# Performance work log

Hardware: AMD Instinct MI355X
Metric: run time of the kernel (lower is better)

Reference implementation:

```python
import jax, jax.numpy as jnp
import numpy as np

EPS = 1e-6

def _ln(x, w, b):
    m = x.mean(-1, keepdims=True)
    v = ((x - m) ** 2).mean(-1, keepdims=True)
    return (x - m) / jnp.sqrt(v + EPS) * w + b

def setup_inputs() -> dict:
    key = jax.random.key(0)
    ks = jax.random.split(key, 16)
    N, P, C, M = 8192, 64, 128, 4096
    MW = M * P  # 262144 gathered tokens
    A, BL = 131072, 65536
    x = jax.random.normal(ks[0], (N, P, C), dtype=jnp.float32)
    index_window = jax.random.permutation(ks[1], N)[:M]
    index_partition = jax.random.permutation(ks[2], MW)
    perm2 = jax.random.permutation(ks[3], MW)
    asy_index = perm2[:A]
    blocked_index = perm2[A:A + BL]
    p = lambda k, sh: 0.02 * jax.random.normal(k, sh, dtype=jnp.float32)
    return {
        "x": x,
        "index_window": index_window,
        "index_partition": index_partition,
        "asy_index": asy_index,
        "blocked_index": blocked_index,
        "M": M,
        "B": N,
        "ln1_w": jnp.ones((C,), jnp.float32), "ln1_b": jnp.zeros((C,), jnp.float32),
        "qkv_w": p(ks[4], (C, 3 * C)), "qkv_b": jnp.zeros((3 * C,), jnp.float32),
        "proj_w": p(ks[5], (C, C)), "proj_b": jnp.zeros((C,), jnp.float32),
        "gamma1": jnp.full((C,), 1e-1, jnp.float32),
        "ln2_w": jnp.ones((C,), jnp.float32), "ln2_b": jnp.zeros((C,), jnp.float32),
        "mlp_w1": p(ks[6], (C, 4 * C)), "mlp_b1": jnp.zeros((4 * C,), jnp.float32),
        "mlp_w2": p(ks[7], (4 * C, C)), "mlp_b2": jnp.zeros((C,), jnp.float32),
        "gamma2": jnp.full((C,), 1e-1, jnp.float32),
    }

def reference(x, index_window, index_partition, asy_index, blocked_index, M, B,
              ln1_w, ln1_b, qkv_w, qkv_b, proj_w, proj_b, gamma1,
              ln2_w, ln2_b, mlp_w1, mlp_b1, mlp_w2, mlp_b2, gamma2):
    N, P, C = x.shape
    H, dh = 4, 32
    scale = dh ** -0.5
    MW = index_partition.shape[0]
    x = _ln(x, ln1_w, ln1_b)                      # first_norm over whole input
    X = x                                          # (N, P, C)
    xw = x[index_window].reshape(-1, C)            # gather windows -> (MW, C)
    XX = xw
    xa = _ln(xw[asy_index], ln1_w, ln1_b)          # second norm on asy tokens
    xw = xw.at[asy_index].set(xa)
    shortcut = xa                                  # (A, C)
    xp = xw[index_partition].reshape(M, -1, C)     # (M, P, C) attention groups
    qkv = (xp @ qkv_w + qkv_b).reshape(M, P, H, 3 * dh).transpose(0, 2, 1, 3)
    q, k, v = jnp.split(qkv, 3, axis=3)            # each (M, H, P, dh)
    attn = jnp.einsum('mhqd,mhkd->mhqk', q, k) * scale
    # scatter scores keyed by key-token into flat map, mask blocked keys, gather back
    am = jnp.zeros((MW, P, H), attn.dtype)
    am = am.at[index_partition].set(jnp.transpose(attn, (0, 3, 2, 1)).reshape(MW, P, H))
    am = am.at[blocked_index].set(-10000.0)
    attn = jnp.transpose(am[index_partition].reshape(M, P, P, H), (0, 3, 2, 1))
    attn = jax.nn.softmax(attn, axis=-1)
    o = jnp.einsum('mhqk,mhkd->mhqd', attn, v).transpose(0, 2, 1, 3).reshape(M, P, C)
    o = o @ proj_w + proj_b
    XX = XX.at[index_partition].set(o.reshape(-1, C))
    y = XX[asy_index]
    # sub_layers: [ls1, droppath(id), ln2, mlp, ls2, droppath(id)]
    y = y * gamma1                                 # i=0
    y = shortcut + y                               # i=1 residual
    shortcut = y
    y2 = _ln(y, ln2_w, ln2_b)                      # i=2
    y2 = jax.nn.gelu(y2 @ mlp_w1 + mlp_b1, approximate=False) @ mlp_w2 + mlp_b2  # i=3
    y2 = y2 * gamma2                               # i=4
    y = shortcut + y2                              # i=5 residual
    XX = XX.at[asy_index].set(y)
    XX = XX.at[blocked_index].set(X[index_window].reshape(-1, C)[blocked_index])
    X = X.at[index_window].set(XX.reshape(M, -1, C))
    return X
```

## Files before the change

kernel.cpp:

```cpp
#include <hip/hip_runtime.h>
#include <hip/hip_bf16.h>
#include <math.h>

#define N_   8192
#define P_   64
#define C_   128
#define M_   4096
#define MW_  (M_ * P_)
#define A_   131072
#define BL_  65536
#define NROWS_ (N_ * P_)
#define LNBLK_   (NROWS_ / 8)
#define PREPBLK_ (196608 / 256)
#define SETBLK_  (MW_ / 256)

typedef __attribute__((ext_vector_type(8))) __bf16 bf16x8;
typedef __attribute__((ext_vector_type(4))) __bf16 bf16x4;
typedef __attribute__((ext_vector_type(4))) float f32x4;
typedef __attribute__((ext_vector_type(2))) __bf16 bf16x2;

__device__ __forceinline__ float wave_sum(float v) {
#pragma unroll
  for (int o = 32; o > 0; o >>= 1) v += __shfl_xor(v, o, 64);
  return v;
}
__device__ __forceinline__ float half_sum(float v) {
#pragma unroll
  for (int o = 1; o < 32; o <<= 1) v += __shfl_xor(v, o, 64);
  return v;
}

__global__ __launch_bounds__(256) void k_scatter2(unsigned char* p,
                                                  const int* __restrict__ ia,
                                                  const int* __restrict__ ib) {
  int i = blockIdx.x * 256 + threadIdx.x;
  if (i < A_) p[ia[i]] = 1;
  else {
    int j = i - A_;
    if (j < BL_) p[ib[j]] = 2;
  }
}

__global__ __launch_bounds__(256) void k_ln_prep_set(
    const float* __restrict__ x,
    const float* __restrict__ w, const float* __restrict__ b,
    const float* __restrict__ qkvw, const float* __restrict__ projw,
    const float* __restrict__ w1, const float* __restrict__ w2,
    __bf16* __restrict__ qkvt, __bf16* __restrict__ projt,
    __bf16* __restrict__ w1t, __bf16* __restrict__ w2t,
    unsigned char* __restrict__ flags,
    float* __restrict__ out) {
  if (blockIdx.x >= LNBLK_) {
    int bx = blockIdx.x - LNBLK_;
    if (bx >= PREPBLK_) {
      int i = (bx - PREPBLK_) * 256 + threadIdx.x;
      flags[i] = 0;
      return;
    }
    int i = bx * 256 + threadIdx.x;
    if (i < 384 * 128) {
      int col = i >> 7, row = i & 127;
      qkvt[i] = (__bf16)qkvw[row * 384 + col];
    } else if (i < 384 * 128 + 128 * 128) {
      int j = i - 384 * 128;
      int col = j >> 7, row = j & 127;
      projt[j] = (__bf16)projw[row * 128 + col];
    } else if (i < 384 * 128 + 128 * 128 + 512 * 128) {
      int j = i - 384 * 128 - 128 * 128;
      int col = j >> 7, row = j & 127;
      w1t[j] = (__bf16)w1[row * 512 + col];
    } else {
      int j = i - 384 * 128 - 128 * 128 - 512 * 128;
      int col = j >> 9, row = j & 511;
      w2t[j] = (__bf16)w2[row * 128 + col];
    }
    return;
  }
  int hw = threadIdx.x >> 5, l = threadIdx.x & 31;
  size_t row = (size_t)blockIdx.x * 8 + hw;
  float4 v = ((const float4*)(x + row * 128))[l];
  float s = (v.x + v.y) + (v.z + v.w);
#pragma unroll
  for (int o = 1; o < 32; o <<= 1) s += __shfl_xor(s, o, 64);
  float mean = s * (1.0f / 128.0f);
  float d0 = v.x - mean, d1 = v.y - mean, d2 = v.z - mean, d3 = v.w - mean;
  float q = (d0 * d0 + d1 * d1) + (d2 * d2 + d3 * d3);
#pragma unroll
  for (int o = 1; o < 32; o <<= 1) q += __shfl_xor(q, o, 64);
  float inv = rsqrtf(q * (1.0f / 128.0f) + 1e-6f);
  float4 wv = ((const float4*)w)[l];
  float4 bv = ((const float4*)b)[l];
  float4 o4;
  o4.x = d0 * inv * wv.x + bv.x;
  o4.y = d1 * inv * wv.y + bv.y;
  o4.z = d2 * inv * wv.z + bv.z;
  o4.w = d3 * inv * wv.w + bv.w;
  ((float4*)(out + row * 128))[l] = o4;
}

__global__ __launch_bounds__(256, 3) void k_attn(
    const int* __restrict__ iw,
    const int* __restrict__ ip, const unsigned char* __restrict__ flags,
    const float* __restrict__ ln1w, const float* __restrict__ ln1b,
    const __bf16* __restrict__ qkvt, const float* __restrict__ qkvb,
    const __bf16* __restrict__ projt, const float* __restrict__ projb,
    float* out) {
  __shared__ __align__(16) __bf16 XV[64 * 132];
  __shared__ __align__(16) __bf16 scratch[4 * 4352];
  __shared__ int srow[64];
  __shared__ unsigned char fl[64];

  const int tid = threadIdx.x;
  const int w = tid >> 6, lane = tid & 63;
  const int quad = lane >> 4, cl = lane & 15;
  const int half = lane >> 5, l32 = lane & 31;
  const int m = blockIdx.x;

  if (tid < 64) {
    int s = ip[(m << 6) + tid];
    fl[tid] = flags[s];
    srow[tid] = iw[s >> 6] * 64 + (s & 63);
  }
  __syncthreads();

  __bf16* Xs = XV;

  {
    const float4 lw4 = ((const float4*)ln1w)[l32];
    const float4 lb4 = ((const float4*)ln1b)[l32];
    float4 xv[8];
#pragma unroll
    for (int ii = 0; ii < 8; ++ii) {
      int r = w * 16 + ii * 2 + half;
      xv[ii] = ((const float4*)(out + (size_t)srow[r] * 128))[l32];
    }
#pragma unroll
    for (int ii = 0; ii < 8; ++ii) {
      int r = w * 16 + ii * 2 + half;
      float4 v = xv[ii];
      if (fl[r] == 1) {
        float mean = half_sum((v.x + v.y) + (v.z + v.w)) * (1.0f / 128.0f);
        float d0 = v.x - mean, d1 = v.y - mean, d2 = v.z - mean, d3 = v.w - mean;
        float inv = rsqrtf(half_sum((d0 * d0 + d1 * d1) + (d2 * d2 + d3 * d3)) *
                               (1.0f / 128.0f) + 1e-6f);
        v.x = d0 * inv * lw4.x + lb4.x;
        v.y = d1 * inv * lw4.y + lb4.y;
        v.z = d2 * inv * lw4.z + lb4.z;
        v.w = d3 * inv * lw4.w + lb4.w;
      }
      bf16x4 p4;
      p4[0] = (__bf16)v.x; p4[1] = (__bf16)v.y;
      p4[2] = (__bf16)v.z; p4[3] = (__bf16)v.w;
      *(bf16x4*)&Xs[r * 132 + l32 * 4] = p4;
    }
  }
  __syncthreads();

  __bf16* wsc = scratch + w * 4352;
  __bf16* Qs  = wsc;
  __bf16* Ks  = wsc + 2176;
  __bf16* Vts = XV + w * 2112;
  __bf16* Ps  = wsc;
  __bf16* Os  = wsc;
  const int h = w;

  bf16x8 af[4][4];
#pragma unroll
  for (int mt = 0; mt < 4; ++mt)
#pragma unroll
    for (int kt = 0; kt < 4; ++kt)
      af[mt][kt] = *(const bf16x8*)&Xs[(mt * 16 + cl) * 132 + kt * 32 + quad * 8];
  __syncthreads();

#pragma unroll
  for (int t = 0; t < 3; ++t) {
#pragma unroll
    for (int nt = 0; nt < 2; ++nt) {
      int col = h * 96 + t * 32 + nt * 16 + cl;
      bf16x8 bfr[4];
#pragma unroll
      for (int kt = 0; kt < 4; ++kt)
        bfr[kt] = *(const bf16x8*)&qkvt[(size_t)col * 128 + kt * 32 + quad * 8];
      float bias = qkvb[col];
      __builtin_amdgcn_s_setprio(1);
#pragma unroll
      for (int mt = 0; mt < 4; ++mt) {
        f32x4 acc = {bias, bias, bias, bias};
#pragma unroll
        for (int kt = 0; kt < 4; ++kt)
          acc = __builtin_amdgcn_mfma_f32_16x16x32_bf16(af[mt][kt], bfr[kt], acc, 0, 0, 0);
        if (t == 0) {
#pragma unroll
          for (int r = 0; r < 4; ++r)
            Qs[(mt * 16 + quad * 4 + r) * 34 + nt * 16 + cl] = (__bf16)acc[r];
        } else if (t == 1) {
#pragma unroll
          for (int r = 0; r < 4; ++r)
            Ks[(mt * 16 + quad * 4 + r) * 34 + nt * 16 + cl] = (__bf16)acc[r];
        } else {
#pragma unroll
          for (int r = 0; r < 4; ++r)
            Vts[(nt * 16 + cl) * 66 + mt * 16 + quad * 4 + r] = (__bf16)acc[r];
        }
      }
      __builtin_amdgcn_s_setprio(0);
    }
  }

  f32x4 sc4[4][4];
  {
    bf16x8 bk[4];
#pragma unroll
    for (int nt = 0; nt < 4; ++nt)
      bk[nt] = *(const bf16x8*)&Ks[(nt * 16 + cl) * 34 + quad * 8];
    __builtin_amdgcn_s_setprio(1);
#pragma unroll
    for (int mt = 0; mt < 4; ++mt) {
      bf16x8 aq = *(const bf16x8*)&Qs[(mt * 16 + cl) * 34 + quad * 8];
#pragma unroll
      for (int nt = 0; nt < 4; ++nt) {
        f32x4 z = {0.f, 0.f, 0.f, 0.f};
        sc4[mt][nt] = __builtin_amdgcn_mfma_f32_16x16x32_bf16(aq, bk[nt], z, 0, 0, 0);
      }
    }
    __builtin_amdgcn_s_setprio(0);
  }
  const float scale = 0.17677669529663687f;
  bool blk[4];
#pragma unroll
  for (int nt = 0; nt < 4; ++nt) blk[nt] = (fl[nt * 16 + cl] == 2);
#pragma unroll
  for (int mt = 0; mt < 4; ++mt)
#pragma unroll
    for (int nt = 0; nt < 4; ++nt)
#pragma unroll
      for (int r = 0; r < 4; ++r) {
        float v = sc4[mt][nt][r];
        sc4[mt][nt][r] = blk[nt] ? -10000.0f : v * scale;
      }
#pragma unroll
  for (int mt = 0; mt < 4; ++mt) {
#pragma unroll
    for (int r = 0; r < 4; ++r) {
      float mx = fmaxf(fmaxf(sc4[mt][0][r], sc4[mt][1][r]),
                       fmaxf(sc4[mt][2][r], sc4[mt][3][r]));
#pragma unroll
      for (int off = 1; off < 16; off <<= 1) mx = fmaxf(mx, __shfl_xor(mx, off, 64));
      float e0 = __expf(sc4[mt][0][r] - mx);
      float e1 = __expf(sc4[mt][1][r] - mx);
      float e2 = __expf(sc4[mt][2][r] - mx);
      float e3 = __expf(sc4[mt][3][r] - mx);
      float sm = (e0 + e1) + (e2 + e3);
#pragma unroll
      for (int off = 1; off < 16; off <<= 1) sm += __shfl_xor(sm, off, 64);
      float inv = 1.0f / sm;
      int row = mt * 16 + quad * 4 + r;
      Ps[row * 68 +  0 + cl] = (__bf16)(e0 * inv);
      Ps[row * 68 + 16 + cl] = (__bf16)(e1 * inv);
      Ps[row * 68 + 32 + cl] = (__bf16)(e2 * inv);
      Ps[row * 68 + 48 + cl] = (__bf16)(e3 * inv);
    }
  }

  f32x4 oacc[4][2];
  {
    bf16x8 bv[2][2];
#pragma unroll
    for (int nt = 0; nt < 2; ++nt)
#pragma unroll
      for (int kt = 0; kt < 2; ++kt)
        bv[nt][kt] = *(const bf16x8*)&Vts[(nt * 16 + cl) * 66 + kt * 32 + quad * 8];
    __builtin_amdgcn_s_setprio(1);
#pragma unroll
    for (int mt = 0; mt < 4; ++mt) {
      bf16x8 ap0 = *(const bf16x8*)&Ps[(mt * 16 + cl) * 68 + quad * 8];
      bf16x8 ap1 = *(const bf16x8*)&Ps[(mt * 16 + cl) * 68 + 32 + quad * 8];
#pragma unroll
      for (int nt = 0; nt < 2; ++nt) {
        f32x4 z = {0.f, 0.f, 0.f, 0.f};
        z = __builtin_amdgcn_mfma_f32_16x16x32_bf16(ap0, bv[nt][0], z, 0, 0, 0);
        z = __builtin_amdgcn_mfma_f32_16x16x32_bf16(ap1, bv[nt][1], z, 0, 0, 0);
        oacc[mt][nt] = z;
      }
    }
    __builtin_amdgcn_s_setprio(0);
  }
#pragma unroll
  for (int mt = 0; mt < 4; ++mt)
#pragma unroll
    for (int nt = 0; nt < 2; ++nt)
#pragma unroll
      for (int r = 0; r < 4; ++r)
        Os[(mt * 16 + quad * 4 + r) * 36 + nt * 16 + cl] = (__bf16)oacc[mt][nt][r];
  __syncthreads();

  const int jw = w * 32;
#pragma unroll
  for (int mt = 0; mt < 4; ++mt) {
#pragma unroll
    for (int nt = 0; nt < 2; ++nt) {
      int col = jw + nt * 16 + cl;
      float pb = projb[col];
      f32x4 acc = {pb, pb, pb, pb};
#pragma unroll
      for (int kt = 0; kt < 4; ++kt) {
        const __bf16* op = scratch + kt * 4352;
        bf16x8 a = *(const bf16x8*)&op[(mt * 16 + cl) * 36 + quad * 8];
        bf16x8 bb = *(const bf16x8*)&projt[(size_t)col * 128 + kt * 32 + quad * 8];
        acc = __builtin_amdgcn_mfma_f32_16x16x32_bf16(a, bb, acc, 0, 0, 0);
      }
#pragma unroll
      for (int r = 0; r < 4; ++r) {
        int row = mt * 16 + quad * 4 + r;
        if (fl[row] != 2)
          out[(size_t)srow[row] * 128 + col] = acc[r];
      }
    }
  }
}

__global__ __launch_bounds__(256, 5) void k_mlp(
    const float* __restrict__ x, const int* __restrict__ iw,
    const int* __restrict__ ia,
    const float* __restrict__ ln1w, const float* __restrict__ ln1b,
    const float* __restrict__ g1,
    const float* __restrict__ ln2w, const float* __restrict__ ln2b,
    const __bf16* __restrict__ w1t, const float* __restrict__ b1,
    const __bf16* __restrict__ w2t, const float* __restrict__ b2,
    const float* __restrict__ g2,
    float* out) {
  __shared__ __align__(16) __bf16 y2s[64 * 136];
  __shared__ __align__(16) __bf16 hb[64 * 68];
  __shared__ int wrs[64];

  const int tid = threadIdx.x;
  const int w = tid >> 6, lane = tid & 63;
  const int quad = lane >> 4, cl = lane & 15;
  const int half = lane >> 5, l32 = lane & 31;

  if (tid < 64) {
    int s = ia[(blockIdx.x << 6) + tid];
    wrs[tid] = iw[s >> 6] * 64 + (s & 63);
  }
  __syncthreads();

  const float4 lw4 = ((const float4*)ln1w)[l32];
  const float4 lb4 = ((const float4*)ln1b)[l32];
  const float4 g14 = ((const float4*)g1)[l32];
  const float4 l2w4 = ((const float4*)ln2w)[l32];
  const float4 l2b4 = ((const float4*)ln2b)[l32];

  for (int qb = 0; qb < 2; ++qb) {
    float4 xv[4], ov[4];
#pragma unroll
    for (int ii = 0; ii < 4; ++ii) {
      int r = w * 16 + (qb * 4 + ii) * 2 + half;
      size_t wr = (size_t)wrs[r];
      xv[ii] = ((const float4*)(x + wr * 128))[l32];
      ov[ii] = ((const float4*)(out + wr * 128))[l32];
    }
#pragma unroll
    for (int ii = 0; ii < 4; ++ii) {
      int r = w * 16 + (qb * 4 + ii) * 2 + half;
      float4 v = xv[ii];
      float mean = half_sum((v.x + v.y) + (v.z + v.w)) * (1.0f / 128.0f);
      float d0 = v.x - mean, d1 = v.y - mean, d2 = v.z - mean, d3 = v.w - mean;
      float inv = rsqrtf(half_sum((d0 * d0 + d1 * d1) + (d2 * d2 + d3 * d3)) *
                             (1.0f / 128.0f) + 1e-6f);
      float y0 = d0 * inv * lw4.x + lb4.x;
      float y1 = d1 * inv * lw4.y + lb4.y;
      float y2 = d2 * inv * lw4.z + lb4.z;
      float y3 = d3 * inv * lw4.w + lb4.w;
      mean = half_sum((y0 + y1) + (y2 + y3)) * (1.0f / 128.0f);
      d0 = y0 - mean; d1 = y1 - mean; d2 = y2 - mean; d3 = y3 - mean;
      inv = rsqrtf(half_sum((d0 * d0 + d1 * d1) + (d2 * d2 + d3 * d3)) *
                       (1.0f / 128.0f) + 1e-6f);
      float4 yv;
      yv.x = (d0 * inv * lw4.x + lb4.x) + g14.x * ov[ii].x;
      yv.y = (d1 * inv * lw4.y + lb4.y) + g14.y * ov[ii].y;
      yv.z = (d2 * inv * lw4.z + lb4.z) + g14.z * ov[ii].z;
      yv.w = (d3 * inv * lw4.w + lb4.w) + g14.w * ov[ii].w;
      ((float4*)(out + (size_t)wrs[r] * 128))[l32] = yv;
      mean = half_sum((yv.x + yv.y) + (yv.z + yv.w)) * (1.0f / 128.0f);
      d0 = yv.x - mean; d1 = yv.y - mean; d2 = yv.z - mean; d3 = yv.w - mean;
      inv = rsqrtf(half_sum((d0 * d0 + d1 * d1) + (d2 * d2 + d3 * d3)) *
                       (1.0f / 128.0f) + 1e-6f);
      bf16x4 p4;
      p4[0] = (__bf16)(d0 * inv * l2w4.x + l2b4.x);
      p4[1] = (__bf16)(d1 * inv * l2w4.y + l2b4.y);
      p4[2] = (__bf16)(d2 * inv * l2w4.z + l2b4.z);
      p4[3] = (__bf16)(d3 * inv * l2w4.w + l2b4.w);
      *(bf16x4*)&y2s[r * 136 + l32 * 4] = p4;
    }
  }
  __threadfence_block();
  __syncthreads();

  f32x4 zacc[4][2];
#pragma unroll
  for (int nt = 0; nt < 2; ++nt) {
    float bb = b2[w * 32 + nt * 16 + cl];
#pragma unroll
    for (int mt = 0; mt < 4; ++mt) zacc[mt][nt] = (f32x4){bb, bb, bb, bb};
  }

  for (int ch = 0; ch < 8; ++ch) {
    {
      int col = ch * 64 + w * 16 + cl;
      bf16x8 bfr[4];
#pragma unroll
      for (int kt = 0; kt < 4; ++kt)
        bfr[kt] = *(const bf16x8*)&w1t[(size_t)col * 128 + kt * 32 + quad * 8];
      float bias = b1[col];
      __builtin_amdgcn_s_setprio(1);
#pragma unroll
      for (int mt = 0; mt < 4; ++mt) {
        f32x4 acc = {bias, bias, bias, bias};
#pragma unroll
        for (int kt = 0; kt < 4; ++kt) {
          bf16x8 a = *(const bf16x8*)&y2s[(mt * 16 + cl) * 136 + kt * 32 + quad * 8];
          acc = __builtin_amdgcn_mfma_f32_16x16x32_bf16(a, bfr[kt], acc, 0, 0, 0);
        }
#pragma unroll
        for (int r = 0; r < 4; ++r) {
          float a = acc[r];
          float g = a * 0.5f * (1.0f + erff(a * 0.70710678118654752f));
          hb[(mt * 16 + quad * 4 + r) * 68 + w * 16 + cl] = (__bf16)g;
        }
      }
      __builtin_amdgcn_s_setprio(0);
    }
    __syncthreads();
#pragma unroll
    for (int nt = 0; nt < 2; ++nt) {
      int col = w * 32 + nt * 16 + cl;
      bf16x8 bfr[2];
#pragma unroll
      for (int kk = 0; kk < 2; ++kk)
        bfr[kk] = *(const bf16x8*)&w2t[(size_t)col * 512 + ch * 64 + kk * 32 + quad * 8];
      __builtin_amdgcn_s_setprio(1);
#pragma unroll
      for (int mt = 0; mt < 4; ++mt)
#pragma unroll
        for (int kk = 0; kk < 2; ++kk) {
          bf16x8 a = *(const bf16x8*)&hb[(mt * 16 + cl) * 68 + kk * 32 + quad * 8];
          zacc[mt][nt] = __builtin_amdgcn_mfma_f32_16x16x32_bf16(a, bfr[kk],
                                                                zacc[mt][nt], 0, 0, 0);
        }
      __builtin_amdgcn_s_setprio(0);
    }
    __syncthreads();
  }

#pragma unroll
  for (int mt = 0; mt < 4; ++mt)
#pragma unroll
    for (int nt = 0; nt < 2; ++nt) {
      int col = w * 32 + nt * 16 + cl;
      float gg = g2[col];
#pragma unroll
      for (int r = 0; r < 4; ++r) {
        int row = mt * 16 + quad * 4 + r;
        size_t a = (size_t)wrs[row] * 128 + col;
        out[a] = out[a] + gg * zacc[mt][nt][r];
      }
    }
}

extern "C" void kernel_launch(void* const* d_in, const int* in_sizes, int n_in,
                              void* d_out, int out_size, void* d_ws, size_t ws_size,
                              hipStream_t stream) {
  const float* x = (const float*)d_in[0];
  const int* iw = (const int*)d_in[1];
  const int* ip = (const int*)d_in[2];
  const int* ia = (const int*)d_in[3];
  const int* ib = (const int*)d_in[4];
  const float* ln1w = (const float*)d_in[7];
  const float* ln1b = (const float*)d_in[8];
  const float* qkvw = (const float*)d_in[9];
  const float* qkvb = (const float*)d_in[10];
  const float* projw = (const float*)d_in[11];
  const float* projb = (const float*)d_in[12];
  const float* g1 = (const float*)d_in[13];
  const float* ln2w = (const float*)d_in[14];
  const float* ln2b = (const float*)d_in[15];
  const float* w1 = (const float*)d_in[16];
  const float* b1 = (const float*)d_in[17];
  const float* w2 = (const float*)d_in[18];
  const float* b2 = (const float*)d_in[19];
  const float* g2 = (const float*)d_in[20];
  float* out = (float*)d_out;

  unsigned char* flags = (unsigned char*)d_ws;
  __bf16* qkvt = (__bf16*)((char*)d_ws + MW_);
  __bf16* projt = (__bf16*)((char*)d_ws + MW_ + 384 * 128 * 2);
  __bf16* w1t = (__bf16*)((char*)d_ws + MW_ + 384 * 128 * 2 + 128 * 128 * 2);
  __bf16* w2t = (__bf16*)((char*)d_ws + MW_ + 384 * 128 * 2 + 128 * 128 * 2 + 512 * 128 * 2);

  k_ln_prep_set<<<LNBLK_ + PREPBLK_ + SETBLK_, 256, 0, stream>>>(
      x, ln1w, ln1b, qkvw, projw, w1, w2, qkvt, projt, w1t, w2t, flags, out);
  k_scatter2<<<(A_ + BL_) / 256, 256, 0, stream>>>(flags, ia, ib);
  k_attn<<<M_, 256, 0, stream>>>(iw, ip, flags, ln1w, ln1b, qkvt, qkvb,
                                 projt, projb, out);
  k_mlp<<<A_ / 64, 256, 0, stream>>>(x, iw, ia, ln1w, ln1b, g1, ln2w, ln2b,
                                     w1t, b1, w2t, b2, g2, out);
}
```

Before: 770.6 us.

## Process two windows per attention block with prefetch of next window's rows

```diff
diff --git a/kernel.cpp b/kernel.cpp
--- a/kernel.cpp
+++ b/kernel.cpp
@@ -28,6 +28,13 @@
 #pragma unroll
   for (int o = 1; o < 32; o <<= 1) v += __shfl_xor(v, o, 64);
   return v;
+}
+
+__device__ __forceinline__ void bar_lds() {
+  __builtin_amdgcn_sched_barrier(0);
+  asm volatile("s_waitcnt lgkmcnt(0)" ::: "memory");
+  __builtin_amdgcn_s_barrier();
+  __builtin_amdgcn_sched_barrier(0);
 }
 
 __global__ __launch_bounds__(256) void k_scatter2(unsigned char* p,
@@ -107,38 +114,43 @@
     float* out) {
   __shared__ __align__(16) __bf16 XV[64 * 132];
   __shared__ __align__(16) __bf16 scratch[4 * 4352];
-  __shared__ int srow[64];
-  __shared__ unsigned char fl[64];
+  __shared__ int srow[2][64];
+  __shared__ unsigned char fl[2][64];
 
   const int tid = threadIdx.x;
   const int w = tid >> 6, lane = tid & 63;
   const int quad = lane >> 4, cl = lane & 15;
   const int half = lane >> 5, l32 = lane & 31;
-  const int m = blockIdx.x;
+  const int m0 = blockIdx.x * 2;
+
+  const float4 lw4 = ((const float4*)ln1w)[l32];
+  const float4 lb4 = ((const float4*)ln1b)[l32];
 
   if (tid < 64) {
-    int s = ip[(m << 6) + tid];
-    fl[tid] = flags[s];
-    srow[tid] = iw[s >> 6] * 64 + (s & 63);
-  }
-  __syncthreads();
-
-  __bf16* Xs = XV;
-
-  {
-    const float4 lw4 = ((const float4*)ln1w)[l32];
-    const float4 lb4 = ((const float4*)ln1b)[l32];
-    float4 xv[8];
-#pragma unroll
-    for (int ii = 0; ii < 8; ++ii) {
-      int r = w * 16 + ii * 2 + half;
-      xv[ii] = ((const float4*)(out + (size_t)srow[r] * 128))[l32];
-    }
+    int s = ip[(m0 << 6) + tid];
+    fl[0][tid] = flags[s];
+    srow[0][tid] = iw[s >> 6] * 64 + (s & 63);
+  }
+  bar_lds();
+
+  float4 xv[8];
+#pragma unroll
+  for (int ii = 0; ii < 8; ++ii) {
+    int r = w * 16 + ii * 2 + half;
+    xv[ii] = ((const float4*)(out + (size_t)srow[0][r] * 128))[l32];
+  }
+
+  for (int it = 0; it < 2; ++it) {
+    const int cur = it, nxt = it ^ 1;
+    const int* src = srow[cur];
+    const unsigned char* flc = fl[cur];
+    __bf16* Xs = XV;
+
 #pragma unroll
     for (int ii = 0; ii < 8; ++ii) {
       int r = w * 16 + ii * 2 + half;
       float4 v = xv[ii];
-      if (fl[r] == 1) {
+      if (flc[r] == 1) {
         float mean = half_sum((v.x + v.y) + (v.z + v.w)) * (1.0f / 128.0f);
         float d0 = v.x - mean, d1 = v.y - mean, d2 = v.z - mean, d3 = v.w - mean;
         float inv = rsqrtf(half_sum((d0 * d0 + d1 * d1) + (d2 * d2 + d3 * d3)) *
@@ -153,169 +165,186 @@
       p4[2] = (__bf16)v.z; p4[3] = (__bf16)v.w;
       *(bf16x4*)&Xs[r * 132 + l32 * 4] = p4;
     }
-  }
-  __syncthreads();
-
-  __bf16* wsc = scratch + w * 4352;
-  __bf16* Qs  = wsc;
-  __bf16* Ks  = wsc + 2176;
-  __bf16* Vts = XV + w * 2112;
-  __bf16* Ps  = wsc;
-  __bf16* Os  = wsc;
-  const int h = w;
-
-  bf16x8 af[4][4];
-#pragma unroll
-  for (int mt = 0; mt < 4; ++mt)
-#pragma unroll
-    for (int kt = 0; kt < 4; ++kt)
-      af[mt][kt] = *(const bf16x8*)&Xs[(mt * 16 + cl) * 132 + kt * 32 + quad * 8];
-  __syncthreads();
-
-#pragma unroll
-  for (int t = 0; t < 3; ++t) {
-#pragma unroll
-    for (int nt = 0; nt < 2; ++nt) {
-      int col = h * 96 + t * 32 + nt * 16 + cl;
-      bf16x8 bfr[4];
+    bar_lds();
+
+    __bf16* wsc = scratch + w * 4352;
+    __bf16* Qs  = wsc;
+    __bf16* Ks  = wsc + 2176;
+    __bf16* Vts = XV + w * 2112;
+    __bf16* Ps  = wsc;
+    __bf16* Os  = wsc;
+    const int h = w;
+
+    bf16x8 af[4][4];
+#pragma unroll
+    for (int mt = 0; mt < 4; ++mt)
 #pragma unroll
       for (int kt = 0; kt < 4; ++kt)
-        bfr[kt] = *(const bf16x8*)&qkvt[(size_t)col * 128 + kt * 32 + quad * 8];
-      float bias = qkvb[col];
+        af[mt][kt] = *(const bf16x8*)&Xs[(mt * 16 + cl) * 132 + kt * 32 + quad * 8];
+
+    int sn = 0;
+    if (it == 0 && tid < 64) sn = ip[((m0 + 1) << 6) + tid];
+    bar_lds();
+
+#pragma unroll
+    for (int t = 0; t < 3; ++t) {
+#pragma unroll
+      for (int nt = 0; nt < 2; ++nt) {
+        int col = h * 96 + t * 32 + nt * 16 + cl;
+        bf16x8 bfr[4];
+#pragma unroll
+        for (int kt = 0; kt < 4; ++kt)
+          bfr[kt] = *(const bf16x8*)&qkvt[(size_t)col * 128 + kt * 32 + quad * 8];
+        float bias = qkvb[col];
+        __builtin_amdgcn_s_setprio(1);
+#pragma unroll
+        for (int mt = 0; mt < 4; ++mt) {
+          f32x4 acc = {bias, bias, bias, bias};
+#pragma unroll
+          for (int kt = 0; kt < 4; ++kt)
+            acc = __builtin_amdgcn_mfma_f32_16x16x32_bf16(af[mt][kt], bfr[kt], acc, 0, 0, 0);
+          if (t == 0) {
+#pragma unroll
+            for (int r = 0; r < 4; ++r)
+              Qs[(mt * 16 + quad * 4 + r) * 34 + nt * 16 + cl] = (__bf16)acc[r];
+          } else if (t == 1) {
+#pragma unroll
+            for (int r = 0; r < 4; ++r)
+              Ks[(mt * 16 + quad * 4 + r) * 34 + nt * 16 + cl] = (__bf16)acc[r];
+          } else {
+#pragma unroll
+            for (int r = 0; r < 4; ++r)
+              Vts[(nt * 16 + cl) * 66 + mt * 16 + quad * 4 + r] = (__bf16)acc[r];
+          }
+        }
+        __builtin_amdgcn_s_setprio(0);
+      }
+    }
+
+    if (it == 0 && tid < 64) {
+      fl[nxt][tid] = flags[sn];
+      srow[nxt][tid] = iw[sn >> 6] * 64 + (sn & 63);
+    }
+
+    f32x4 sc4[4][4];
+    {
+      bf16x8 bk[4];
+#pragma unroll
+      for (int nt = 0; nt < 4; ++nt)
+        bk[nt] = *(const bf16x8*)&Ks[(nt * 16 + cl) * 34 + quad * 8];
       __builtin_amdgcn_s_setprio(1);
 #pragma unroll
       for (int mt = 0; mt < 4; ++mt) {
-        f32x4 acc = {bias, bias, bias, bias};
-#pragma unroll
-        for (int kt = 0; kt < 4; ++kt)
-          acc = __builtin_amdgcn_mfma_f32_16x16x32_bf16(af[mt][kt], bfr[kt], acc, 0, 0, 0);
-        if (t == 0) {
-#pragma unroll
-          for (int r = 0; r < 4; ++r)
-            Qs[(mt * 16 + quad * 4 + r) * 34 + nt * 16 + cl] = (__bf16)acc[r];
-        } else if (t == 1) {
-#pragma unroll
-          for (int r = 0; r < 4; ++r)
-            Ks[(mt * 16 + quad * 4 + r) * 34 + nt * 16 + cl] = (__bf16)acc[r];
-        } else {
-#pragma unroll
-          for (int r = 0; r < 4; ++r)
-            Vts[(nt * 16 + cl) * 66 + mt * 16 + quad * 4 + r] = (__bf16)acc[r];
+        bf16x8 aq = *(const bf16x8*)&Qs[(mt * 16 + cl) * 34 + quad * 8];
+#pragma unroll
+        for (int nt = 0; nt < 4; ++nt) {
+          f32x4 z = {0.f, 0.f, 0.f, 0.f};
+          sc4[mt][nt] = __builtin_amdgcn_mfma_f32_16x16x32_bf16(aq, bk[nt], z, 0, 0, 0);
         }
       }
       __builtin_amdgcn_s_setprio(0);
     }
-  }
-
-  f32x4 sc4[4][4];
-  {
-    bf16x8 bk[4];
-#pragma unroll
-    for (int nt = 0; nt < 4; ++nt)
-      bk[nt] = *(const bf16x8*)&Ks[(nt * 16 + cl) * 34 + quad * 8];
-    __builtin_amdgcn_s_setprio(1);
+    const float scale = 0.17677669529663687f;
+    bool blk[4];
+#pragma unroll
+    for (int nt = 0; nt < 4; ++nt) blk[nt] = (flc[nt * 16 + cl] == 2);
+#pragma unroll
+    for (int mt = 0; mt < 4; ++mt)
+#pragma unroll
+      for (int nt = 0; nt < 4; ++nt)
+#pragma unroll
+        for (int r = 0; r < 4; ++r) {
+          float v = sc4[mt][nt][r];
+          sc4[mt][nt][r] = blk[nt] ? -10000.0f : v * scale;
+        }
 #pragma unroll
     for (int mt = 0; mt < 4; ++mt) {
-      bf16x8 aq = *(const bf16x8*)&Qs[(mt * 16 + cl) * 34 + quad * 8];
-#pragma unroll
-      for (int nt = 0; nt < 4; ++nt) {
-        f32x4 z = {0.f, 0.f, 0.f, 0.f};
-        sc4[mt][nt] = __builtin_amdgcn_mfma_f32_16x16x32_bf16(aq, bk[nt], z, 0, 0, 0);
-      }
-    }
-    __builtin_amdgcn_s_setprio(0);
-  }
-  const float scale = 0.17677669529663687f;
-  bool blk[4];
-#pragma unroll
-  for (int nt = 0; nt < 4; ++nt) blk[nt] = (fl[nt * 16 + cl] == 2);
-#pragma unroll
-  for (int mt = 0; mt < 4; ++mt)
-#pragma unroll
-    for (int nt = 0; nt < 4; ++nt)
 #pragma unroll
       for (int r = 0; r < 4; ++r) {
-        float v = sc4[mt][nt][r];
-        sc4[mt][nt][r] = blk[nt] ? -10000.0f : v * scale;
-      }
-#pragma unroll
-  for (int mt = 0; mt < 4; ++mt) {
-#pragma unroll
-    for (int r = 0; r < 4; ++r) {
-      float mx = fmaxf(fmaxf(sc4[mt][0][r], sc4[mt][1][r]),
-                       fmaxf(sc4[mt][2][r], sc4[mt][3][r]));
-#pragma unroll
-      for (int off = 1; off < 16; off <<= 1) mx = fmaxf(mx, __shfl_xor(mx, off, 64));
-      float e0 = __expf(sc4[mt][0][r] - mx);
-      float e1 = __expf(sc4[mt][1][r] - mx);
-      float e2 = __expf(sc4[mt][2][r] - mx);
-      float e3 = __expf(sc4[mt][3][r] - mx);
-      float sm = (e0 + e1) + (e2 + e3);
-#pragma unroll
-      for (int off = 1; off < 16; off <<= 1) sm += __shfl_xor(sm, off, 64);
-      float inv = 1.0f / sm;
-      int row = mt * 16 + quad * 4 + r;
-      Ps[row * 68 +  0 + cl] = (__bf16)(e0 * inv);
-      Ps[row * 68 + 16 + cl] = (__bf16)(e1 * inv);
-      Ps[row * 68 + 32 + cl] = (__bf16)(e2 * inv);
-      Ps[row * 68 + 48 + cl] = (__bf16)(e3 * inv);
-    }
-  }
-
-  f32x4 oacc[4][2];
-  {
-    bf16x8 bv[2][2];
-#pragma unroll
-    for (int nt = 0; nt < 2; ++nt)
-#pragma unroll
-      for (int kt = 0; kt < 2; ++kt)
-        bv[nt][kt] = *(const bf16x8*)&Vts[(nt * 16 + cl) * 66 + kt * 32 + quad * 8];
-    __builtin_amdgcn_s_setprio(1);
+        float mx = fmaxf(fmaxf(sc4[mt][0][r], sc4[mt][1][r]),
+                         fmaxf(sc4[mt][2][r], sc4[mt][3][r]));
+#pragma unroll
+        for (int off = 1; off < 16; off <<= 1) mx = fmaxf(mx, __shfl_xor(mx, off, 64));
+        float e0 = __expf(sc4[mt][0][r] - mx);
+        float e1 = __expf(sc4[mt][1][r] - mx);
+        float e2 = __expf(sc4[mt][2][r] - mx);
+        float e3 = __expf(sc4[mt][3][r] - mx);
+        float sm = (e0 + e1) + (e2 + e3);
+#pragma unroll
+        for (int off = 1; off < 16; off <<= 1) sm += __shfl_xor(sm, off, 64);
+        float inv = 1.0f / sm;
+        int row = mt * 16 + quad * 4 + r;
+        Ps[row * 68 +  0 + cl] = (__bf16)(e0 * inv);
+        Ps[row * 68 + 16 + cl] = (__bf16)(e1 * inv);
+        Ps[row * 68 + 32 + cl] = (__bf16)(e2 * inv);
+        Ps[row * 68 + 48 + cl] = (__bf16)(e3 * inv);
+      }
+    }
+
+    f32x4 oacc[4][2];
+    {
+      bf16x8 bv[2][2];
+#pragma unroll
+      for (int nt = 0; nt < 2; ++nt)
+#pragma unroll
+        for (int kt = 0; kt < 2; ++kt)
+          bv[nt][kt] = *(const bf16x8*)&Vts[(nt * 16 + cl) * 66 + kt * 32 + quad * 8];
+      __builtin_amdgcn_s_setprio(1);
+#pragma unroll
+      for (int mt = 0; mt < 4; ++mt) {
+        bf16x8 ap0 = *(const bf16x8*)&Ps[(mt * 16 + cl) * 68 + quad * 8];
+        bf16x8 ap1 = *(const bf16x8*)&Ps[(mt * 16 + cl) * 68 + 32 + quad * 8];
+#pragma unroll
+        for (int nt = 0; nt < 2; ++nt) {
+          f32x4 z = {0.f, 0.f, 0.f, 0.f};
+          z = __builtin_amdgcn_mfma_f32_16x16x32_bf16(ap0, bv[nt][0], z, 0, 0, 0);
+          z = __builtin_amdgcn_mfma_f32_16x16x32_bf16(ap1, bv[nt][1], z, 0, 0, 0);
+          oacc[mt][nt] = z;
+        }
+      }
+      __builtin_amdgcn_s_setprio(0);
+    }
+#pragma unroll
+    for (int mt = 0; mt < 4; ++mt)
+#pragma unroll
+      for (int nt = 0; nt < 2; ++nt)
+#pragma unroll
+        for (int r = 0; r < 4; ++r)
+          Os[(mt * 16 + quad * 4 + r) * 36 + nt * 16 + cl] = (__bf16)oacc[mt][nt][r];
+    bar_lds();
+
+    if (it == 0) {
+#pragma unroll
+      for (int ii = 0; ii < 8; ++ii) {
+        int r = w * 16 + ii * 2 + half;
+        xv[ii] = ((const float4*)(out + (size_t)srow[nxt][r] * 128))[l32];
+      }
+    }
+
+    const int jw = w * 32;
 #pragma unroll
     for (int mt = 0; mt < 4; ++mt) {
-      bf16x8 ap0 = *(const bf16x8*)&Ps[(mt * 16 + cl) * 68 + quad * 8];
-      bf16x8 ap1 = *(const bf16x8*)&Ps[(mt * 16 + cl) * 68 + 32 + quad * 8];
 #pragma unroll
       for (int nt = 0; nt < 2; ++nt) {
-        f32x4 z = {0.f, 0.f, 0.f, 0.f};
-        z = __builtin_amdgcn_mfma_f32_16x16x32_bf16(ap0, bv[nt][0], z, 0, 0, 0);
-        z = __builtin_amdgcn_mfma_f32_16x16x32_bf16(ap1, bv[nt][1], z, 0, 0, 0);
-        oacc[mt][nt] = z;
-      }
-    }
-    __builtin_amdgcn_s_setprio(0);
-  }
-#pragma unroll
-  for (int mt = 0; mt < 4; ++mt)
-#pragma unroll
-    for (int nt = 0; nt < 2; ++nt)
-#pragma unroll
-      for (int r = 0; r < 4; ++r)
-        Os[(mt * 16 + quad * 4 + r) * 36 + nt * 16 + cl] = (__bf16)oacc[mt][nt][r];
-  __syncthreads();
-
-  const int jw = w * 32;
-#pragma unroll
-  for (int mt = 0; mt < 4; ++mt) {
-#pragma unroll
-    for (int nt = 0; nt < 2; ++nt) {
-      int col = jw + nt * 16 + cl;
-      float pb = projb[col];
-      f32x4 acc = {pb, pb, pb, pb};
-#pragma unroll
-      for (int kt = 0; kt < 4; ++kt) {
-        const __bf16* op = scratch + kt * 4352;
-        bf16x8 a = *(const bf16x8*)&op[(mt * 16 + cl) * 36 + quad * 8];
-        bf16x8 bb = *(const bf16x8*)&projt[(size_t)col * 128 + kt * 32 + quad * 8];
-        acc = __builtin_amdgcn_mfma_f32_16x16x32_bf16(a, bb, acc, 0, 0, 0);
-      }
-#pragma unroll
-      for (int r = 0; r < 4; ++r) {
-        int row = mt * 16 + quad * 4 + r;
-        if (fl[row] != 2)
-          out[(size_t)srow[row] * 128 + col] = acc[r];
-      }
-    }
+        int col = jw + nt * 16 + cl;
+        float pb = projb[col];
+        f32x4 acc = {pb, pb, pb, pb};
+#pragma unroll
+        for (int kt = 0; kt < 4; ++kt) {
+          const __bf16* op = scratch + kt * 4352;
+          bf16x8 a = *(const bf16x8*)&op[(mt * 16 + cl) * 36 + quad * 8];
+          bf16x8 bb = *(const bf16x8*)&projt[(size_t)col * 128 + kt * 32 + quad * 8];
+          acc = __builtin_amdgcn_mfma_f32_16x16x32_bf16(a, bb, acc, 0, 0, 0);
+        }
+#pragma unroll
+        for (int r = 0; r < 4; ++r) {
+          int row = mt * 16 + quad * 4 + r;
+          if (flc[row] != 2)
+            out[(size_t)src[row] * 128 + col] = acc[r];
+        }
+      }
+    }
+    bar_lds();
   }
 }
 
@@ -500,8 +529,8 @@
   k_ln_prep_set<<<LNBLK_ + PREPBLK_ + SETBLK_, 256, 0, stream>>>(
       x, ln1w, ln1b, qkvw, projw, w1, w2, qkvt, projt, w1t, w2t, flags, out);
   k_scatter2<<<(A_ + BL_) / 256, 256, 0, stream>>>(flags, ia, ib);
-  k_attn<<<M_, 256, 0, stream>>>(iw, ip, flags, ln1w, ln1b, qkvt, qkvb,
-                                 projt, projb, out);
+  k_attn<<<M_ / 2, 256, 0, stream>>>(iw, ip, flags, ln1w, ln1b, qkvt, qkvb,
+                                     projt, projb, out);
   k_mlp<<<A_ / 64, 256, 0, stream>>>(x, iw, ia, ln1w, ln1b, g1, ln2w, ln2b,
                                      w1t, b1, w2t, b2, g2, out);
 }
```

Result: slower. 861.6 us (+11.8%).
